# Kernel optimization log

Measured on AMD Instinct MI355X. Metric: run time of the kernel, lower is better.

## Reference

```python
import jax, jax.numpy as jnp
import numpy as np

D_IN = 1024
D_OUT = 1024
NUM_HEADS = 16
DIM_HEAD = D_OUT // NUM_HEADS


def setup_inputs() -> dict:
    key = jax.random.key(0)
    ks = jax.random.split(key, 6)
    s = 0.02
    x = jax.random.normal(ks[0], (2, 2048, D_IN), dtype=jnp.float32)
    Wk = jax.random.normal(ks[1], (D_IN, D_OUT), dtype=jnp.float32) * s
    Wq = jax.random.normal(ks[2], (D_IN, D_OUT), dtype=jnp.float32) * s
    Wv = jax.random.normal(ks[3], (D_IN, D_OUT), dtype=jnp.float32) * s
    Wo = jax.random.normal(ks[4], (D_OUT, D_OUT), dtype=jnp.float32) * s
    bo = jax.random.normal(ks[5], (D_OUT,), dtype=jnp.float32) * s
    return {"x": x, "Wk": Wk, "Wq": Wq, "Wv": Wv, "Wo": Wo, "bo": bo}


def reference(x, Wk, Wq, Wv, Wo, bo):
    B, S, _ = x.shape
    # projections -> [B, H, S, Dh]
    def split_heads(t):
        return t.reshape(B, S, NUM_HEADS, DIM_HEAD).transpose(0, 2, 1, 3)
    q = split_heads(x @ Wq)
    k = split_heads(x @ Wk)
    v = split_heads(x @ Wv)
    # NOTE: source uses non-in-place masked_fill whose result is discarded,
    # so NO causal mask is actually applied (faithful reproduction).
    scores = jnp.einsum("bhqd,bhkd->bhqk", q, k) / jnp.sqrt(jnp.float32(DIM_HEAD))
    wgts = jax.nn.softmax(scores, axis=-1)  # dropout = identity (eval mode)
    ctx = jnp.einsum("bhqk,bhkd->bhqd", wgts, v)
    ctx = ctx.transpose(0, 2, 1, 3).reshape(B, S, D_OUT)
    return ctx @ Wo + bo
```

## Files before the change

kernel.cpp:

```cpp
#include <hip/hip_runtime.h>
#include <stdint.h>

typedef short bf16x8 __attribute__((ext_vector_type(8)));
typedef float f32x4  __attribute__((ext_vector_type(4)));
typedef unsigned int u32x4 __attribute__((ext_vector_type(4)));
typedef unsigned int u32x2 __attribute__((ext_vector_type(2)));

__device__ __forceinline__ unsigned short f2bf(float f) {
  unsigned int u = __builtin_bit_cast(unsigned int, f) + 0x8000u;
  return (unsigned short)(u >> 16);
}
__device__ __forceinline__ unsigned int pack2bf(float a, float b) {
  unsigned int ua = __builtin_bit_cast(unsigned int, a) + 0x8000u;
  unsigned int ub = __builtin_bit_cast(unsigned int, b) + 0x8000u;
  return __builtin_amdgcn_perm(ub, ua, 0x07060302);
}
__device__ __forceinline__ unsigned int cvtpk2bf(float a, float b) {
  unsigned int r;
  asm("v_cvt_pk_bf16_f32 %0, %1, %2" : "=v"(r) : "v"(a), "v"(b));
  return r;
}

__device__ __forceinline__ void gl2lds16(const void* g, void* l) {
  __builtin_amdgcn_global_load_lds(
      (const __attribute__((address_space(1))) void*)g,
      (__attribute__((address_space(3))) void*)l, 16, 0, 0);
}

template <int N> __device__ __forceinline__ void wait_vmcnt() {
  asm volatile("s_waitcnt vmcnt(%0)" ::"n"(N) : "memory");
}

__global__ __launch_bounds__(256) void cast_fused_k(
    const float* __restrict__ x, unsigned short* __restrict__ xb,
    const float* __restrict__ Wq, const float* __restrict__ Wk,
    const float* __restrict__ Wv, const float* __restrict__ Wo,
    unsigned short* __restrict__ Tq, unsigned short* __restrict__ Tk,
    unsigned short* __restrict__ Tv, unsigned short* __restrict__ To) {
  __shared__ float tile[32][33];
  const int tid = threadIdx.x;
  const int bid = blockIdx.x;
  if (bid < 4096) {
    int i = bid * 256 + tid;
    float4 v = ((const float4*)x)[i];
    u32x2 o;
    o.x = pack2bf(v.x, v.y);
    o.y = pack2bf(v.z, v.w);
    ((u32x2*)xb)[i] = o;
  } else {
    const int bb = bid - 4096;
    const int z = bb >> 10, rem = bb & 1023;
    const float* W = (z == 0) ? Wq : (z == 1) ? Wk : (z == 2) ? Wv : Wo;
    unsigned short* T = (z == 0) ? Tq : (z == 1) ? Tk : (z == 2) ? Tv : To;
    const int tx = tid & 31, ty = tid >> 5;
    const int n0 = (rem & 31) * 32, k0 = (rem >> 5) * 32;
#pragma unroll
    for (int j = 0; j < 32; j += 8)
      tile[ty + j][tx] = W[(size_t)(k0 + ty + j) * 1024 + n0 + tx];
    __syncthreads();
#pragma unroll
    for (int j = 0; j < 32; j += 8)
      T[(size_t)(n0 + ty + j) * 1024 + k0 + tx] = f2bf(tile[tx][ty + j]);
  }
}

template <int MODE, int TN, int WN, int NTHR>
__global__ __launch_bounds__(NTHR, 2) void gemm_bt_k(const unsigned short* __restrict__ A,
                                                     const unsigned short* __restrict__ B,
                                                     void* __restrict__ C,
                                                     const float* __restrict__ bias,
                                                     int K) {
  constexpr int BN = WN * TN * 16;
  constexpr int ALD = 512 / NTHR;
  constexpr int BLD = BN * 4 / NTHR;
  constexpr int PT = ALD + BLD;
  __shared__ alignas(16) short lA[4][512 * 8];
  __shared__ alignas(16) short lB[4][BN * 4 * 8];
  const int tid = threadIdx.x;
  const int wid = tid >> 6, lane = tid & 63;
  const int l15 = lane & 15, quad = lane >> 4;
  const int waveM = wid / WN, waveN = wid % WN;
  const int bm = blockIdx.y * 128, bn = blockIdx.x * BN;

  f32x4 acc[4][TN];
#pragma unroll
  for (int i = 0; i < 4; ++i)
#pragma unroll
    for (int j = 0; j < TN; ++j) acc[i][j] = (f32x4){0.f, 0.f, 0.f, 0.f};

  auto stage = [&](int kk, short* la, short* lb) {
#pragma unroll
    for (int j = 0; j < ALD; ++j) {
      int c = tid + NTHR * j;
      int row = ((c >> 6) << 4) | (c & 15);
      int ch = (c >> 4) & 3;
      gl2lds16(A + (size_t)(bm + row) * K + kk + ch * 8, &la[(c & ~63) * 8]);
    }
#pragma unroll
    for (int j = 0; j < BLD; ++j) {
      int c = tid + NTHR * j;
      int row = ((c >> 6) << 4) | (c & 15);
      int ch = (c >> 4) & 3;
      gl2lds16(B + (size_t)(bn + row) * K + kk + ch * 8, &lb[(c & ~63) * 8]);
    }
  };

  auto compute = [&](const short* la, const short* lb) {
    bf16x8 af[4], bfr[TN];
#pragma unroll
    for (int i = 0; i < 4; ++i)
      af[i] = *(const bf16x8*)&la[(((waveM * 4 + i) * 64) + lane) * 8];
#pragma unroll
    for (int j = 0; j < TN; ++j)
      bfr[j] = *(const bf16x8*)&lb[(((waveN * TN + j) * 64) + lane) * 8];
    __builtin_amdgcn_s_setprio(1);
#pragma unroll
    for (int i = 0; i < 4; ++i)
#pragma unroll
      for (int j = 0; j < TN; ++j)
        acc[i][j] = __builtin_amdgcn_mfma_f32_16x16x32_bf16(af[i], bfr[j], acc[i][j], 0, 0, 0);
    __builtin_amdgcn_s_setprio(0);
  };

  const int NT = K >> 5;
  short *pa0 = lA[0], *pa1 = lA[1], *pa2 = lA[2], *pa3 = lA[3];
  short *pb0 = lB[0], *pb1 = lB[1], *pb2 = lB[2], *pb3 = lB[3];
  stage(0, pa0, pb0);
  stage(32, pa1, pb1);
#pragma unroll 1
  for (int t = 0; t < NT - 2; ++t) {
    stage((t + 2) * 32, pa2, pb2);
    wait_vmcnt<2 * PT>();
    __builtin_amdgcn_sched_barrier(0);
    __builtin_amdgcn_s_barrier();
    __builtin_amdgcn_sched_barrier(0);
    compute(pa0, pb0);
    short* ta = pa0; pa0 = pa1; pa1 = pa2; pa2 = pa3; pa3 = ta;
    short* tb = pb0; pb0 = pb1; pb1 = pb2; pb2 = pb3; pb3 = tb;
  }
  wait_vmcnt<PT>();
  __builtin_amdgcn_sched_barrier(0);
  __builtin_amdgcn_s_barrier();
  __builtin_amdgcn_sched_barrier(0);
  compute(pa0, pb0);
  { short* ta = pa0; pa0 = pa1; pa1 = pa2; pa2 = pa3; pa3 = ta;
    short* tb = pb0; pb0 = pb1; pb1 = pb2; pb2 = pb3; pb3 = tb; }
  wait_vmcnt<0>();
  __builtin_amdgcn_sched_barrier(0);
  __builtin_amdgcn_s_barrier();
  __builtin_amdgcn_sched_barrier(0);
  compute(pa0, pb0);

#pragma unroll
  for (int i = 0; i < 4; ++i)
#pragma unroll
    for (int j = 0; j < TN; ++j) {
      int row = bm + waveM * 64 + i * 16 + quad * 4;
      int col = bn + (waveN * TN + j) * 16 + l15;
      if (MODE == 0) {
        unsigned short* Cq = (unsigned short*)C;
        int w = col >> 10, n1 = col & 1023;
        int h = n1 >> 6, d = n1 & 63;
        int b = row >> 11, s = row & 2047;
        int bhh = (b << 4) + h;
        if (w == 2) {
          int g = (i << 2) + quad;
          int ks2 = g >> 3, rem = g & 7;
          int pos = ((ks2 << 2) + (rem & 3)) * 8 + (rem >> 2) * 4;
          u32x2 pk;
          pk.x = pack2bf(acc[i][j][0], acc[i][j][1]);
          pk.y = pack2bf(acc[i][j][2], acc[i][j][3]);
          *(u32x2*)&Cq[(size_t)2 * 4194304 + ((size_t)bhh * 64 + d) * 2048 +
                       (s & ~63) + pos] = pk;
        } else {
          float sc = (w == 0) ? 0.18033688011112042f : 1.0f;
#pragma unroll
          for (int r = 0; r < 4; ++r)
            Cq[(size_t)w * 4194304 + ((size_t)bhh * 2048 + s + r) * 64 + d] =
                f2bf(acc[i][j][r] * sc);
        }
      } else {
#pragma unroll
        for (int r = 0; r < 4; ++r)
          ((float*)C)[(size_t)(row + r) * 1024 + col] = acc[i][j][r] + bias[col];
      }
    }
}

__global__ __launch_bounds__(256, 2) void flash_k(const unsigned short* __restrict__ Qh,
                                                  const unsigned short* __restrict__ Kh,
                                                  const unsigned short* __restrict__ Vt,
                                                  unsigned short* __restrict__ ctxb) {
  constexpr int SL = 2048;
  __shared__ alignas(16) short kt[4][512 * 8];
  __shared__ alignas(16) short vt[4][512 * 8];

  const int tid = threadIdx.x;
  const int wid = tid >> 6, lane = tid & 63;
  const int l15 = lane & 15, quad = lane >> 4;
  const int bid = blockIdx.x;
  const int jj = bid >> 3;
  const int bh = ((bid & 7) << 2) | (jj >> 4);
  const int q0 = (jj & 15) * 128 + wid * 32;

  const unsigned short* Qb = Qh + (size_t)bh * SL * 64;
  const unsigned short* Kb = Kh + (size_t)bh * SL * 64;
  const unsigned short* Vb = Vt + (size_t)bh * 64 * SL;

  bf16x8 qf[2][2];
#pragma unroll
  for (int s = 0; s < 2; ++s)
#pragma unroll
    for (int ks = 0; ks < 2; ++ks)
      qf[s][ks] = *(const bf16x8*)(Qb + (size_t)(q0 + s * 16 + l15) * 64 + ks * 32 + quad * 8);

  f32x4 o[2][4];
  f32x4 rs4[2] = {(f32x4){0.f, 0.f, 0.f, 0.f}, (f32x4){0.f, 0.f, 0.f, 0.f}};
  const f32x4 z4 = (f32x4){0.f, 0.f, 0.f, 0.f};
#pragma unroll
  for (int s = 0; s < 2; ++s)
#pragma unroll
    for (int t = 0; t < 4; ++t) o[s][t] = z4;

  auto stage = [&](int kb, short* ktb, short* vtb) {
#pragma unroll
    for (int j2 = 0; j2 < 2; ++j2) {
      int cc = tid + 256 * j2;
      int row = cc >> 3;
      int ko = (cc & 7) ^ (row & 7);
      gl2lds16(Kb + (size_t)(kb + row) * 64 + ko * 8, &ktb[(cc & ~63) * 8]);
      gl2lds16(Vb + (size_t)row * SL + kb + ko * 8, &vtb[(cc & ~63) * 8]);
    }
  };

  auto computeQK = [&](const short* ktb, f32x4 (&sv)[2][4]) {
    __builtin_amdgcn_s_setprio(1);
#pragma unroll
    for (int t = 0; t < 4; ++t) {
      int key = t * 16 + l15;
      bf16x8 kf0 = *(bf16x8*)&ktb[(key * 8 + (quad ^ (key & 7))) * 8];
      bf16x8 kf1 = *(bf16x8*)&ktb[(key * 8 + ((4 + quad) ^ (key & 7))) * 8];
#pragma unroll
      for (int s = 0; s < 2; ++s) {
        sv[s][t] = __builtin_amdgcn_mfma_f32_16x16x32_bf16(kf0, qf[s][0], z4, 0, 0, 0);
        sv[s][t] = __builtin_amdgcn_mfma_f32_16x16x32_bf16(kf1, qf[s][1], sv[s][t], 0, 0, 0);
      }
    }
    __builtin_amdgcn_s_setprio(0);
  };

  auto computeSMPV = [&](const short* vtb, f32x4 (&sv)[2][4]) {
    u32x4 pf[2][2];
#pragma unroll
    for (int s = 0; s < 2; ++s)
#pragma unroll
      for (int t = 0; t < 4; ++t) {
        f32x4 p;
#pragma unroll
        for (int r = 0; r < 4; ++r) p[r] = __builtin_amdgcn_exp2f(sv[s][t][r]);
        rs4[s] += p;
        pf[s][t >> 1][(t & 1) * 2 + 0] = cvtpk2bf(p[0], p[1]);
        pf[s][t >> 1][(t & 1) * 2 + 1] = cvtpk2bf(p[2], p[3]);
      }
    __builtin_amdgcn_s_setprio(1);
#pragma unroll
    for (int t = 0; t < 4; ++t) {
      int d = t * 16 + l15;
#pragma unroll
      for (int ks = 0; ks < 2; ++ks) {
        bf16x8 vf = *(bf16x8*)&vtb[(d * 8 + ((ks * 4 + quad) ^ (d & 7))) * 8];
#pragma unroll
        for (int s = 0; s < 2; ++s)
          o[s][t] = __builtin_amdgcn_mfma_f32_16x16x32_bf16(
              vf, __builtin_bit_cast(bf16x8, pf[s][ks]), o[s][t], 0, 0, 0);
      }
    }
    __builtin_amdgcn_s_setprio(0);
  };

  short *kA0 = kt[0], *kA1 = kt[1], *kB0 = kt[2], *kB1 = kt[3];
  short *vA0 = vt[0], *vA1 = vt[1], *vB0 = vt[2], *vB1 = vt[3];
  stage(0, kA0, vA0);
  stage(64, kA1, vA1);
#pragma unroll 1
  for (int i2 = 0; i2 < 16; ++i2) {
    wait_vmcnt<0>();
    __builtin_amdgcn_sched_barrier(0);
    __builtin_amdgcn_s_barrier();
    __builtin_amdgcn_sched_barrier(0);
    if (i2 < 15) {
      stage((2 * i2 + 2) * 64, kB0, vB0);
      stage((2 * i2 + 3) * 64, kB1, vB1);
    }
    f32x4 sv0[2][4], sv1[2][4];
    computeQK(kA0, sv0);
    computeQK(kA1, sv1);
    computeSMPV(vA0, sv0);
    computeSMPV(vA1, sv1);
    short* t;
    t = kA0; kA0 = kB0; kB0 = t;  t = kA1; kA1 = kB1; kB1 = t;
    t = vA0; vA0 = vB0; vB0 = t;  t = vA1; vA1 = vB1; vB1 = t;
  }

  const int bb = bh >> 4, h = bh & 15;
#pragma unroll
  for (int s = 0; s < 2; ++s) {
    float v = (rs4[s][0] + rs4[s][1]) + (rs4[s][2] + rs4[s][3]);
    v += __shfl_xor(v, 16);
    v += __shfl_xor(v, 32);
    float inv = 1.0f / v;
    int tok = q0 + s * 16 + l15;
    size_t base = ((size_t)(bb * 2048 + tok)) * 1024 + h * 64;
#pragma unroll
    for (int t = 0; t < 4; ++t) {
      u32x2 pk;
      pk.x = pack2bf(o[s][t][0] * inv, o[s][t][1] * inv);
      pk.y = pack2bf(o[s][t][2] * inv, o[s][t][3] * inv);
      *(u32x2*)&ctxb[base + t * 16 + quad * 4] = pk;
    }
  }
}

extern "C" void kernel_launch(void* const* d_in, const int* in_sizes, int n_in,
                              void* d_out, int out_size, void* d_ws, size_t ws_size,
                              hipStream_t stream) {
  const float* x  = (const float*)d_in[0];
  const float* Wk = (const float*)d_in[1];
  const float* Wq = (const float*)d_in[2];
  const float* Wv = (const float*)d_in[3];
  const float* Wo = (const float*)d_in[4];
  const float* bo = (const float*)d_in[5];
  float* out = (float*)d_out;

  char* ws = (char*)d_ws;
  const size_t MB = 1u << 20;
  unsigned short* xb   = (unsigned short*)(ws);
  unsigned short* WqT  = (unsigned short*)(ws + 8  * MB);
  unsigned short* WkT  = (unsigned short*)(ws + 10 * MB);
  unsigned short* WvT  = (unsigned short*)(ws + 12 * MB);
  unsigned short* WoT  = (unsigned short*)(ws + 14 * MB);
  unsigned short* Qh   = (unsigned short*)(ws + 16 * MB);
  unsigned short* ctxb = xb;

  cast_fused_k<<<8192, 256, 0, stream>>>(x, xb, Wq, Wk, Wv, Wo, WqT, WkT, WvT, WoT);
  gemm_bt_k<0, 6, 4, 512><<<dim3(8, 32), 512, 0, stream>>>(xb, WqT, Qh, nullptr, 1024);
  flash_k<<<512, 256, 0, stream>>>(Qh, Qh + 4194304, Qh + 2 * 4194304, ctxb);
  gemm_bt_k<1, 2, 4, 512><<<dim3(8, 32), 512, 0, stream>>>(ctxb, WoT, out, bo, 1024);
}
```

Before: 185.8 us.

## Load K tiles directly from global into registers instead of staging through LDS

The flash attention kernel no longer stages K blocks through shared memory. Each wave now reads its K fragments for both 64-key blocks straight from global memory into registers at the start of each iteration, while V keeps its LDS double buffering. This halves LDS use and removes the LDS reads for K, which could allow higher occupancy. In exchange, all four waves load the same K data redundantly, and the global load latency is exposed right before the QK MFMAs with no prefetch.

```diff
diff --git a/kernel.cpp b/kernel.cpp
--- a/kernel.cpp
+++ b/kernel.cpp
@@ -192,7 +192,6 @@
                                                   const unsigned short* __restrict__ Vt,
                                                   unsigned short* __restrict__ ctxb) {
   constexpr int SL = 2048;
-  __shared__ alignas(16) short kt[4][512 * 8];
   __shared__ alignas(16) short vt[4][512 * 8];
 
   const int tid = threadIdx.x;
@@ -222,28 +221,26 @@
 #pragma unroll
     for (int t = 0; t < 4; ++t) o[s][t] = z4;
 
-  auto stage = [&](int kb, short* ktb, short* vtb) {
+  const unsigned short* Kfb = Kb + (size_t)l15 * 64 + quad * 8;
+
+  auto stageV = [&](int kb, short* vtb) {
 #pragma unroll
     for (int j2 = 0; j2 < 2; ++j2) {
       int cc = tid + 256 * j2;
       int row = cc >> 3;
       int ko = (cc & 7) ^ (row & 7);
-      gl2lds16(Kb + (size_t)(kb + row) * 64 + ko * 8, &ktb[(cc & ~63) * 8]);
       gl2lds16(Vb + (size_t)row * SL + kb + ko * 8, &vtb[(cc & ~63) * 8]);
     }
   };
 
-  auto computeQK = [&](const short* ktb, f32x4 (&sv)[2][4]) {
+  auto computeQKr = [&](const bf16x8* kr, f32x4 (&sv)[2][4]) {
     __builtin_amdgcn_s_setprio(1);
 #pragma unroll
     for (int t = 0; t < 4; ++t) {
-      int key = t * 16 + l15;
-      bf16x8 kf0 = *(bf16x8*)&ktb[(key * 8 + (quad ^ (key & 7))) * 8];
-      bf16x8 kf1 = *(bf16x8*)&ktb[(key * 8 + ((4 + quad) ^ (key & 7))) * 8];
 #pragma unroll
       for (int s = 0; s < 2; ++s) {
-        sv[s][t] = __builtin_amdgcn_mfma_f32_16x16x32_bf16(kf0, qf[s][0], z4, 0, 0, 0);
-        sv[s][t] = __builtin_amdgcn_mfma_f32_16x16x32_bf16(kf1, qf[s][1], sv[s][t], 0, 0, 0);
+        sv[s][t] = __builtin_amdgcn_mfma_f32_16x16x32_bf16(kr[2 * t], qf[s][0], z4, 0, 0, 0);
+        sv[s][t] = __builtin_amdgcn_mfma_f32_16x16x32_bf16(kr[2 * t + 1], qf[s][1], sv[s][t], 0, 0, 0);
       }
     }
     __builtin_amdgcn_s_setprio(0);
@@ -278,27 +275,36 @@
     __builtin_amdgcn_s_setprio(0);
   };
 
-  short *kA0 = kt[0], *kA1 = kt[1], *kB0 = kt[2], *kB1 = kt[3];
   short *vA0 = vt[0], *vA1 = vt[1], *vB0 = vt[2], *vB1 = vt[3];
-  stage(0, kA0, vA0);
-  stage(64, kA1, vA1);
+  stageV(0, vA0);
+  stageV(64, vA1);
 #pragma unroll 1
   for (int i2 = 0; i2 < 16; ++i2) {
     wait_vmcnt<0>();
     __builtin_amdgcn_sched_barrier(0);
     __builtin_amdgcn_s_barrier();
     __builtin_amdgcn_sched_barrier(0);
+    bf16x8 kr0[8], kr1[8];
+    const unsigned short* Ka = Kfb + (size_t)(2 * i2) * 64 * 64;
+#pragma unroll
+    for (int t = 0; t < 4; ++t) {
+      kr0[2 * t]     = *(const bf16x8*)(Ka + (size_t)(t * 16) * 64);
+      kr0[2 * t + 1] = *(const bf16x8*)(Ka + (size_t)(t * 16) * 64 + 32);
+      kr1[2 * t]     = *(const bf16x8*)(Ka + (size_t)(64 + t * 16) * 64);
+      kr1[2 * t + 1] = *(const bf16x8*)(Ka + (size_t)(64 + t * 16) * 64 + 32);
+    }
+    __builtin_amdgcn_sched_barrier(0);
     if (i2 < 15) {
-      stage((2 * i2 + 2) * 64, kB0, vB0);
-      stage((2 * i2 + 3) * 64, kB1, vB1);
-    }
+      stageV((2 * i2 + 2) * 64, vB0);
+      stageV((2 * i2 + 3) * 64, vB1);
+    }
+    __builtin_amdgcn_sched_barrier(0);
     f32x4 sv0[2][4], sv1[2][4];
-    computeQK(kA0, sv0);
-    computeQK(kA1, sv1);
+    computeQKr(kr0, sv0);
+    computeQKr(kr1, sv1);
     computeSMPV(vA0, sv0);
     computeSMPV(vA1, sv1);
     short* t;
-    t = kA0; kA0 = kB0; kB0 = t;  t = kA1; kA1 = kB1; kB1 = t;
     t = vA0; vA0 = vB0; vB0 = t;  t = vA1; vA1 = vB1; vB1 = t;
   }
 
```

Result: slower. 212.8 us (+14.5%).
